# Performance work log

Hardware: AMD Instinct MI355X
Metric: run time of the kernel (lower is better)

The kernel has to match this reference:

```python
import math
import jax, jax.numpy as jnp
import numpy as np

ALPHA = -12.032
MODEL_DIM = 2
CONST_NORM = math.sqrt(MODEL_DIM)
HEAD_DIM = 2
ROPE_PERIOD = 19.0
OMEGA = 2.0 * math.pi / ROPE_PERIOD
PEAK_EPS = 0.3
PHI = OMEGA * (10.0 + PEAK_EPS)
TARGET_LOGIT_GAP = math.log(10.0)
ATTN_AMPLITUDE = TARGET_LOGIT_GAP / (math.cos(OMEGA * PEAK_EPS) - math.cos(OMEGA * (1.0 - PEAK_EPS)))
QK_NORM_SCALE = math.sqrt(ATTN_AMPLITUDE / math.sqrt(2.0))
ATTN_SCALE = HEAD_DIM ** (-0.5) * QK_NORM_SCALE ** 2
S_CONST = 100.0 / 256.0
VOCAB_SIZE = 10
V_FACTOR = -22.0 / CONST_NORM


def _unit_rms_norm(x, eps=1e-6):
    return x * jax.lax.rsqrt(jnp.mean(x * x, axis=-1, keepdims=True) + eps)


def _apply_rope(x):
    # x: [B, 1, S, 2]; rotate the 2-dim pair by pos*OMEGA
    seq_len = x.shape[2]
    theta = jnp.arange(seq_len, dtype=x.dtype) * OMEGA
    cos_t = jnp.cos(theta)[None, None, :, None]
    sin_t = jnp.sin(theta)[None, None, :, None]
    x0, x1 = x[..., 0:1], x[..., 1:2]
    return jnp.concatenate([x0 * cos_t - x1 * sin_t, x0 * sin_t + x1 * cos_t], axis=-1)


def setup_inputs() -> dict:
    key = jax.random.key(0)
    tokens = jax.random.randint(key, (4, 4096), 0, VOCAB_SIZE)
    c = jnp.ones((1,), dtype=jnp.float32)  # learned scalar param (torch init 0 -> NaN; use 1)
    return {"tokens": tokens, "c": c}


def reference(tokens, c):
    cs = c[0]
    d = jnp.arange(VOCAB_SIZE, dtype=jnp.float32)
    tab = jnp.stack([cs - d * d / cs, -d], axis=-1)  # [V, 2]

    h = tab[tokens]  # [B, S, 2]
    seq_len = h.shape[1]
    mask = jnp.triu(jnp.full((seq_len, seq_len), -1e9, dtype=h.dtype), k=1)[None, None]

    # --- attention block ---
    hn = _unit_rms_norm(h)
    x0, x1 = hn[..., 0], hn[..., 1]
    q = jnp.stack([x0 * math.cos(PHI), x0 * -math.sin(PHI)], axis=-1)[:, None]  # [B,1,S,2]
    k = jnp.stack([x0, jnp.zeros_like(x0)], axis=-1)[:, None]
    v = jnp.stack([x1 * (V_FACTOR * cs), jnp.zeros_like(x0)], axis=-1)[:, None]
    q = _apply_rope(_unit_rms_norm(q))
    k = _apply_rope(_unit_rms_norm(k))
    attn = jnp.einsum('bhqd,bhkd->bhqk', q, k) * ATTN_SCALE + mask  # [B,1,S,S]
    attn = jax.nn.softmax(attn, axis=-1)
    o = jnp.einsum('bhqk,bhkd->bhqd', attn, v)[:, 0]  # [B,S,2]
    attn_out = jnp.stack([jnp.zeros_like(o[..., 0]), o[..., 0]], axis=-1)  # o_proj
    h = h + attn_out

    # --- SiLU-gated MLP block ---
    hn = _unit_rms_norm(h)
    a = ALPHA * cs
    gc = 128.0 * cs
    g0 = hn[..., 0] * a + hn[..., 1] * gc
    g1 = hn[..., 0] * (a - gc / cs) + hn[..., 1] * gc
    gate = jnp.stack([g0, g1], axis=-1)
    up = hn[..., 0:1]  # broadcast to INTERMEDIATE_SIZE=2
    mix = jax.nn.silu(gate) * up
    y1 = S_CONST * (mix[..., 1] - mix[..., 0])
    h = h + jnp.stack([jnp.zeros_like(y1), y1], axis=-1)

    # --- final norm + tied output projection ---
    nw = jnp.stack([0.1 * cs / CONST_NORM, -cs / (50.0 * CONST_NORM)])
    out = _unit_rms_norm(h) * nw
    return out @ tab.T  # [B, S, V]
```

## Files before the change

kernel.cpp:

```cpp
#include <hip/hip_runtime.h>
#include <math.h>

#define SEQ 4096
#define RPB 32
#define NSLOT 40

__global__ __launch_bounds__(256) void fused_model(const int* __restrict__ tokens,
                                                   const float* __restrict__ cptr,
                                                   float* __restrict__ out) {
  __shared__ int    cnt[192];
  __shared__ float4 btab[NSLOT];
  __shared__ float4 ktab[RPB];
  __shared__ int    dl[RPB];
  __shared__ float  salpha[10], sv[10], sq0[10], sq1[10];

  const int tid = threadIdx.x;
  const int b = blockIdx.y;
  const int i0 = blockIdx.x * RPB;
  const float cs = cptr[0];

  const double omega_d = 2.0 * M_PI / 19.0;
  const double phi_d = omega_d * 10.3;
  const double amp_d = log(10.0) / (cos(omega_d * 0.3) - cos(omega_d * 0.7));
  const double qkns_d = sqrt(amp_d / sqrt(2.0));
  const double attn_scale_d = (1.0 / sqrt(2.0)) * qkns_d * qkns_d;
  const float omega_f = (float)omega_d;
  const float c1 = (float)cos(phi_d);
  const float ns1 = (float)(-sin(phi_d));
  const float S2 = (float)attn_scale_d * 1.4426950408889634f;
  const float vfac = (float)(-22.0 / sqrt(2.0));

  if (tid < 192) cnt[tid] = 0;
  if (tid < 10) {
    float d = (float)tid;
    float h0 = cs - d * d / cs;
    float h1 = -d;
    float inv = rsqrtf((h0 * h0 + h1 * h1) * 0.5f + 1e-6f);
    float x0 = h0 * inv, x1 = h1 * inv;
    salpha[tid] = x0 * rsqrtf((x0 * x0) * 0.5f + 1e-6f);
    sv[tid] = x1 * (vfac * cs);
    float q0 = x0 * c1, q1 = x0 * ns1;
    float invq = rsqrtf((q0 * q0 + q1 * q1) * 0.5f + 1e-6f);
    sq0[tid] = q0 * invq;
    sq1[tid] = q1 * invq;
  }
  __syncthreads();

  const int* tb = tokens + b * SEQ;

  if (tid < RPB) {
    int j = i0 + tid;
    int d = tb[j];
    float st, ct;
    sincosf((float)j * omega_f, &st, &ct);
    float al = salpha[d];
    ktab[tid] = make_float4(al * ct, al * st, sv[d], 0.f);
    dl[tid] = d;
  }

  for (int base = 0; base < i0; base += 1024) {
    int j4 = base + tid * 4;
    if (j4 < i0) {
      int4 t4 = *reinterpret_cast<const int4*>(tb + j4);
      int r = j4 % 19;
      atomicAdd(&cnt[t4.x * 19 + r], 1); r = (r + 1 < 19) ? r + 1 : 0;
      atomicAdd(&cnt[t4.y * 19 + r], 1); r = (r + 1 < 19) ? r + 1 : 0;
      atomicAdd(&cnt[t4.z * 19 + r], 1); r = (r + 1 < 19) ? r + 1 : 0;
      atomicAdd(&cnt[t4.w * 19 + r], 1);
    }
  }
  __syncthreads();

  if (tid < NSLOT) {
    float C = 0.f, W = 0.f, kx = 0.f, ky = 0.f;
    if (tid < 19) {
      int c = cnt[tid];
      C = (float)c; W = C * sv[0];
      float st, ct; sincosf((float)tid * omega_f, &st, &ct);
      kx = salpha[0] * ct; ky = salpha[0] * st;
    } else if (tid < 38) {
      int r = tid - 19;
      int s = 0; float w = 0.f;
#pragma unroll
      for (int d = 2; d < 10; ++d) { int c = cnt[d * 19 + r]; s += c; w += (float)c * sv[d]; }
      C = (float)s; W = w;
      float st, ct; sincosf((float)r * omega_f, &st, &ct);
      kx = salpha[2] * ct; ky = salpha[2] * st;
    } else if (tid == 38) {
      int s = 0;
#pragma unroll
      for (int r = 0; r < 19; ++r) s += cnt[19 + r];
      C = (float)s; W = C * sv[1];
    }
    btab[tid] = make_float4(kx, ky, C, W);
  }
  __syncthreads();

  const int wid = tid >> 6;
  const int lane = tid & 63;
  const int row = lane & 7;
  const int part = lane >> 3;
  const int tmax = wid * 8 + row;
  const int i = i0 + tmax;
  const int di = dl[tmax];
  float st, ct;
  sincosf((float)i * omega_f, &st, &ct);
  const float qx = (sq0[di] * ct - sq1[di] * st) * S2;
  const float qy = (sq0[di] * st + sq1[di] * ct) * S2;

  float m = -1e30f;
#pragma unroll
  for (int k = 0; k < 5; ++k) {
    float4 t = btab[part + k * 8];
    float l = fmaf(qx, t.x, qy * t.y);
    m = fmaxf(m, (t.z != 0.f) ? l : -1e30f);
  }
#pragma unroll
  for (int k = 0; k < 4; ++k) {
    int t = part + k * 8;
    float4 kk = ktab[t];
    float l = fmaf(qx, kk.x, qy * kk.y);
    m = fmaxf(m, (t <= tmax) ? l : -1e30f);
  }

  float den = 0.f, num = 0.f;
#pragma unroll
  for (int k = 0; k < 5; ++k) {
    float4 t = btab[part + k * 8];
    float l = fmaf(qx, t.x, qy * t.y);
    l = (t.z != 0.f) ? l : -1e30f;
    float e = exp2f(l - m);
    den = fmaf(e, t.z, den);
    num = fmaf(e, t.w, num);
  }
#pragma unroll
  for (int k = 0; k < 4; ++k) {
    int t = part + k * 8;
    float4 kk = ktab[t];
    float l = fmaf(qx, kk.x, qy * kk.y);
    float e = (t <= tmax) ? exp2f(l - m) : 0.f;
    den += e;
    num = fmaf(e, kk.z, num);
  }

#pragma unroll
  for (int off = 8; off < 64; off <<= 1) {
    float mo = __shfl_xor(m, off);
    float dno = __shfl_xor(den, off);
    float nmo = __shfl_xor(num, off);
    float M = fmaxf(m, mo);
    float sa = exp2f(m - M), sb = exp2f(mo - M);
    den = fmaf(den, sa, dno * sb);
    num = fmaf(num, sa, nmo * sb);
    m = M;
  }
  const float o0 = num / den;

  const float df = (float)di;
  const float h0 = cs - df * df / cs;
  const float h1 = -df;
  const float h1a = h1 + o0;
  const float inv2 = rsqrtf((h0 * h0 + h1a * h1a) * 0.5f + 1e-6f);
  const float n0 = h0 * inv2, n1 = h1a * inv2;
  const float aa = -12.032f * cs;
  const float gc = 128.0f * cs;
  const float g0 = n0 * aa + n1 * gc;
  const float g1 = n0 * (aa - gc / cs) + n1 * gc;
  const float m0_ = (g0 / (1.f + expf(-g0))) * n0;
  const float m1_ = (g1 / (1.f + expf(-g1))) * n0;
  const float y1 = 0.390625f * (m1_ - m0_);
  const float h1b = h1a + y1;
  const float inv3 = rsqrtf((h0 * h0 + h1b * h1b) * 0.5f + 1e-6f);
  const float nw0 = (0.1f * cs) / 1.41421356237309515f;
  const float nw1 = -cs / 70.7106781186547524f;
  const float r0 = h0 * inv3 * nw0;
  const float r1 = h1b * inv3 * nw1;

  const size_t ob = (size_t)(b * SEQ + i) * 10;
  {
    float dc = (float)part;
    out[ob + part] = r0 * (cs - dc * dc / cs) + r1 * (-dc);
    if (part < 2) {
      float dc2 = (float)(8 + part);
      out[ob + 8 + part] = r0 * (cs - dc2 * dc2 / cs) + r1 * (-dc2);
    }
  }
}

extern "C" void kernel_launch(void* const* d_in, const int* in_sizes, int n_in,
                              void* d_out, int out_size, void* d_ws, size_t ws_size,
                              hipStream_t stream) {
  const int* tokens = (const int*)d_in[0];
  const float* c = (const float*)d_in[1];
  float* out = (float*)d_out;
  const int batches = in_sizes[0] / SEQ;
  dim3 grid(SEQ / RPB, batches);
  fused_model<<<grid, 256, 0, stream>>>(tokens, c, out);
}
```

Measured before the change: 9.777 us.

## Prefetch tokens early, use hardware sin/cos, and simplify softmax reduction

Token loads for the histogram and the local row are issued at kernel start, before the shared-table setup and barrier, so global memory latency overlaps with that setup. sincosf is replaced by a reduction into revolutions (idx/19) followed by the AMD hardware sin/cos intrinsics, which removes the slow-path range reduction. The online-softmax merge is replaced by a max shuffle-reduce first, then a plain sum reduce of den and num, which cuts the shuffle and exp work in the merge. The trade-offs are higher register pressure from holding four int4 prefetches and slightly lower precision from the hardware trig instructions.

```diff
diff --git a/kernel.cpp b/kernel.cpp
--- a/kernel.cpp
+++ b/kernel.cpp
@@ -4,6 +4,13 @@
 #define SEQ 4096
 #define RPB 32
 #define NSLOT 40
+
+__device__ __forceinline__ void sincos19(float idx, float* s, float* c) {
+  float rev = idx * (1.0f / 19.0f);
+  rev -= floorf(rev);
+  *s = __builtin_amdgcn_sinf(rev);
+  *c = __builtin_amdgcn_cosf(rev);
+}
 
 __global__ __launch_bounds__(256) void fused_model(const int* __restrict__ tokens,
                                                    const float* __restrict__ cptr,
@@ -18,13 +25,23 @@
   const int b = blockIdx.y;
   const int i0 = blockIdx.x * RPB;
   const float cs = cptr[0];
+  const int* tb = tokens + b * SEQ;
+
+  int dloc = 0;
+  if (tid < RPB) dloc = tb[i0 + tid];
+  const int tj = tid * 4;
+  int4 tt[4];
+#pragma unroll
+  for (int it = 0; it < 4; ++it) {
+    int j4 = it * 1024 + tj;
+    if (j4 < i0) tt[it] = *reinterpret_cast<const int4*>(tb + j4);
+  }
 
   const double omega_d = 2.0 * M_PI / 19.0;
   const double phi_d = omega_d * 10.3;
   const double amp_d = log(10.0) / (cos(omega_d * 0.3) - cos(omega_d * 0.7));
   const double qkns_d = sqrt(amp_d / sqrt(2.0));
   const double attn_scale_d = (1.0 / sqrt(2.0)) * qkns_d * qkns_d;
-  const float omega_f = (float)omega_d;
   const float c1 = (float)cos(phi_d);
   const float ns1 = (float)(-sin(phi_d));
   const float S2 = (float)attn_scale_d * 1.4426950408889634f;
@@ -46,27 +63,26 @@
   }
   __syncthreads();
 
-  const int* tb = tokens + b * SEQ;
-
   if (tid < RPB) {
-    int j = i0 + tid;
-    int d = tb[j];
-    float st, ct;
-    sincosf((float)j * omega_f, &st, &ct);
-    float al = salpha[d];
-    ktab[tid] = make_float4(al * ct, al * st, sv[d], 0.f);
-    dl[tid] = d;
-  }
-
-  for (int base = 0; base < i0; base += 1024) {
-    int j4 = base + tid * 4;
-    if (j4 < i0) {
-      int4 t4 = *reinterpret_cast<const int4*>(tb + j4);
-      int r = j4 % 19;
-      atomicAdd(&cnt[t4.x * 19 + r], 1); r = (r + 1 < 19) ? r + 1 : 0;
-      atomicAdd(&cnt[t4.y * 19 + r], 1); r = (r + 1 < 19) ? r + 1 : 0;
-      atomicAdd(&cnt[t4.z * 19 + r], 1); r = (r + 1 < 19) ? r + 1 : 0;
-      atomicAdd(&cnt[t4.w * 19 + r], 1);
+    float sj, cj;
+    sincos19((float)(i0 + tid), &sj, &cj);
+    float al = salpha[dloc];
+    ktab[tid] = make_float4(al * cj, al * sj, sv[dloc], 0.f);
+    dl[tid] = dloc;
+  }
+  {
+    int r = tj % 19;
+#pragma unroll
+    for (int it = 0; it < 4; ++it) {
+      int j4 = it * 1024 + tj;
+      if (j4 < i0) {
+        int q = r;
+        atomicAdd(&cnt[tt[it].x * 19 + q], 1); q = (q + 1 < 19) ? q + 1 : 0;
+        atomicAdd(&cnt[tt[it].y * 19 + q], 1); q = (q + 1 < 19) ? q + 1 : 0;
+        atomicAdd(&cnt[tt[it].z * 19 + q], 1); q = (q + 1 < 19) ? q + 1 : 0;
+        atomicAdd(&cnt[tt[it].w * 19 + q], 1);
+      }
+      r = (r >= 2) ? r - 2 : r + 17;
     }
   }
   __syncthreads();
@@ -76,16 +92,16 @@
     if (tid < 19) {
       int c = cnt[tid];
       C = (float)c; W = C * sv[0];
-      float st, ct; sincosf((float)tid * omega_f, &st, &ct);
-      kx = salpha[0] * ct; ky = salpha[0] * st;
+      float sr, cr; sincos19((float)tid, &sr, &cr);
+      kx = salpha[0] * cr; ky = salpha[0] * sr;
     } else if (tid < 38) {
       int r = tid - 19;
       int s = 0; float w = 0.f;
 #pragma unroll
       for (int d = 2; d < 10; ++d) { int c = cnt[d * 19 + r]; s += c; w += (float)c * sv[d]; }
       C = (float)s; W = w;
-      float st, ct; sincosf((float)r * omega_f, &st, &ct);
-      kx = salpha[2] * ct; ky = salpha[2] * st;
+      float sr, cr; sincos19((float)r, &sr, &cr);
+      kx = salpha[2] * cr; ky = salpha[2] * sr;
     } else if (tid == 38) {
       int s = 0;
 #pragma unroll
@@ -103,56 +119,48 @@
   const int tmax = wid * 8 + row;
   const int i = i0 + tmax;
   const int di = dl[tmax];
-  float st, ct;
-  sincosf((float)i * omega_f, &st, &ct);
-  const float qx = (sq0[di] * ct - sq1[di] * st) * S2;
-  const float qy = (sq0[di] * st + sq1[di] * ct) * S2;
-
-  float m = -1e30f;
-#pragma unroll
-  for (int k = 0; k < 5; ++k) {
-    float4 t = btab[part + k * 8];
-    float l = fmaf(qx, t.x, qy * t.y);
-    m = fmaxf(m, (t.z != 0.f) ? l : -1e30f);
-  }
-#pragma unroll
-  for (int k = 0; k < 4; ++k) {
-    int t = part + k * 8;
-    float4 kk = ktab[t];
-    float l = fmaf(qx, kk.x, qy * kk.y);
-    m = fmaxf(m, (t <= tmax) ? l : -1e30f);
-  }
+  float sti, cti;
+  sincos19((float)i, &sti, &cti);
+  const float qx = (sq0[di] * cti - sq1[di] * sti) * S2;
+  const float qy = (sq0[di] * sti + sq1[di] * cti) * S2;
+
+  float4 sl0 = btab[part], sl1 = btab[part + 8], sl2 = btab[part + 16],
+         sl3 = btab[part + 24], sl4 = btab[part + 32];
+  float4 tl0 = ktab[part], tl1 = ktab[part + 8], tl2 = ktab[part + 16],
+         tl3 = ktab[part + 24];
+
+  float l0 = (sl0.z != 0.f) ? fmaf(qx, sl0.x, qy * sl0.y) : -1e30f;
+  float l1 = (sl1.z != 0.f) ? fmaf(qx, sl1.x, qy * sl1.y) : -1e30f;
+  float l2 = (sl2.z != 0.f) ? fmaf(qx, sl2.x, qy * sl2.y) : -1e30f;
+  float l3 = (sl3.z != 0.f) ? fmaf(qx, sl3.x, qy * sl3.y) : -1e30f;
+  float l4 = (sl4.z != 0.f) ? fmaf(qx, sl4.x, qy * sl4.y) : -1e30f;
+  float t0 = (part      <= tmax) ? fmaf(qx, tl0.x, qy * tl0.y) : -1e30f;
+  float t1 = (part + 8  <= tmax) ? fmaf(qx, tl1.x, qy * tl1.y) : -1e30f;
+  float t2 = (part + 16 <= tmax) ? fmaf(qx, tl2.x, qy * tl2.y) : -1e30f;
+  float t3 = (part + 24 <= tmax) ? fmaf(qx, tl3.x, qy * tl3.y) : -1e30f;
+
+  float m = fmaxf(fmaxf(fmaxf(l0, l1), fmaxf(l2, l3)),
+                  fmaxf(fmaxf(l4, t0), fmaxf(fmaxf(t1, t2), t3)));
+#pragma unroll
+  for (int off = 8; off < 64; off <<= 1) m = fmaxf(m, __shfl_xor(m, off));
 
   float den = 0.f, num = 0.f;
-#pragma unroll
-  for (int k = 0; k < 5; ++k) {
-    float4 t = btab[part + k * 8];
-    float l = fmaf(qx, t.x, qy * t.y);
-    l = (t.z != 0.f) ? l : -1e30f;
-    float e = exp2f(l - m);
-    den = fmaf(e, t.z, den);
-    num = fmaf(e, t.w, num);
-  }
-#pragma unroll
-  for (int k = 0; k < 4; ++k) {
-    int t = part + k * 8;
-    float4 kk = ktab[t];
-    float l = fmaf(qx, kk.x, qy * kk.y);
-    float e = (t <= tmax) ? exp2f(l - m) : 0.f;
-    den += e;
-    num = fmaf(e, kk.z, num);
-  }
-
+  {
+    float e;
+    e = exp2f(l0 - m); den = fmaf(e, sl0.z, den); num = fmaf(e, sl0.w, num);
+    e = exp2f(l1 - m); den = fmaf(e, sl1.z, den); num = fmaf(e, sl1.w, num);
+    e = exp2f(l2 - m); den = fmaf(e, sl2.z, den); num = fmaf(e, sl2.w, num);
+    e = exp2f(l3 - m); den = fmaf(e, sl3.z, den); num = fmaf(e, sl3.w, num);
+    e = exp2f(l4 - m); den = fmaf(e, sl4.z, den); num = fmaf(e, sl4.w, num);
+    e = exp2f(t0 - m); den += e; num = fmaf(e, tl0.z, num);
+    e = exp2f(t1 - m); den += e; num = fmaf(e, tl1.z, num);
+    e = exp2f(t2 - m); den += e; num = fmaf(e, tl2.z, num);
+    e = exp2f(t3 - m); den += e; num = fmaf(e, tl3.z, num);
+  }
 #pragma unroll
   for (int off = 8; off < 64; off <<= 1) {
-    float mo = __shfl_xor(m, off);
-    float dno = __shfl_xor(den, off);
-    float nmo = __shfl_xor(num, off);
-    float M = fmaxf(m, mo);
-    float sa = exp2f(m - M), sb = exp2f(mo - M);
-    den = fmaf(den, sa, dno * sb);
-    num = fmaf(num, sa, nmo * sb);
-    m = M;
+    den += __shfl_xor(den, off);
+    num += __shfl_xor(num, off);
   }
   const float o0 = num / den;
 
```

Measured after the change: 9.753 us. About the same (-0.2%).
